# Performance work log

Hardware: AMD Instinct MI355X
Metric: run time of the kernel (lower is better)

## Reference

```python
import jax, jax.numpy as jnp
import numpy as np
import math

V = 50000; E = 300; H = 512; T = 11; P = 18; L = 2048
NHEAD = 2; NLAYERS = 2; NUM_LSTM_LAYERS = 2; FF = E  # TransformerEncoderLayer dim_feedforward=embedding_dim
START, STOP = 0, 1
NEG = -10000.0


def _mk_lstm_params(key, in_dim, hid):
    ks = jax.random.split(key, 4)
    s = 1.0 / math.sqrt(hid)
    return {
        'Wi': jax.random.uniform(ks[0], (4 * hid, in_dim), minval=-s, maxval=s),
        'Wh': jax.random.uniform(ks[1], (4 * hid, hid), minval=-s, maxval=s),
        'bi': jax.random.uniform(ks[2], (4 * hid,), minval=-s, maxval=s),
        'bh': jax.random.uniform(ks[3], (4 * hid,), minval=-s, maxval=s),
    }


def setup_inputs() -> dict:
    key = jax.random.key(0)
    ks = jax.random.split(key, 32)
    sentence = jax.random.randint(ks[0], (L,), 0, V)
    pos_tagging = jax.random.randint(ks[1], (L,), 0, P)
    tf_idf = jax.random.uniform(ks[2], (L,))
    tags = jax.random.randint(ks[3], (L,), 2, T)  # avoid START/STOP as gold tags

    word_embeds = jax.random.normal(ks[4], (V, E)) * 0.1

    in_dim = E + P + 1
    half = H // 2
    lstm = []
    ki = 5
    for layer in range(NUM_LSTM_LAYERS):
        d = in_dim if layer == 0 else H
        lstm.append({'fwd': _mk_lstm_params(ks[ki], d, half), 'bwd': _mk_lstm_params(ks[ki + 1], d, half)})
        ki += 2
    h0 = jax.random.normal(ks[ki], (2 * NUM_LSTM_LAYERS, half)); ki += 1
    c0 = jax.random.normal(ks[ki], (2 * NUM_LSTM_LAYERS, half)); ki += 1

    def dense(k, o, i):
        s = 1.0 / math.sqrt(i)
        k1, k2 = jax.random.split(k)
        return (jax.random.uniform(k1, (o, i), minval=-s, maxval=s),
                jax.random.uniform(k2, (o,), minval=-s, maxval=s))

    tlayers = []
    for _ in range(NLAYERS):
        kk = jax.random.split(ks[ki], 8); ki += 1
        Wqkv, bqkv = dense(kk[0], 3 * H, H)
        Wo, bo = dense(kk[1], H, H)
        W1, b1 = dense(kk[2], FF, H)
        W2, b2 = dense(kk[3], H, FF)
        tlayers.append({
            'Wqkv': Wqkv, 'bqkv': bqkv, 'Wo': Wo, 'bo': bo,
            'W1': W1, 'b1': b1, 'W2': W2, 'b2': b2,
            'g1': jnp.ones((H,)), 'be1': jnp.zeros((H,)),
            'g2': jnp.ones((H,)), 'be2': jnp.zeros((H,)),
        })

    W_tag, b_tag = dense(ks[ki], T, H); ki += 1
    transitions = jax.random.normal(ks[ki], (T, T))
    transitions = transitions.at[START, :].set(NEG).at[:, STOP].set(NEG)

    # flatten transformer params into named entries
    inp = {
        'sentence': sentence, 'pos_tagging': pos_tagging, 'tf_idf': tf_idf, 'tags': tags,
        'word_embeds': word_embeds, 'h0': h0, 'c0': c0,
        'W_tag': W_tag, 'b_tag': b_tag, 'transitions': transitions,
    }
    for li in range(NUM_LSTM_LAYERS):
        for d in ('fwd', 'bwd'):
            for p in ('Wi', 'Wh', 'bi', 'bh'):
                inp[f'lstm{li}_{d}_{p}'] = lstm[li][d][p]
    for li in range(NLAYERS):
        for p, v in tlayers[li].items():
            inp[f't{li}_{p}'] = v
    return inp


def _lstm_dir(x, p, h0, c0, reverse):
    # x: [L, in_dim]
    def step(carry, xt):
        h, c = carry
        g = p['Wi'] @ xt + p['bi'] + p['Wh'] @ h + p['bh']
        i, f, gg, o = jnp.split(g, 4)
        i = jax.nn.sigmoid(i); f = jax.nn.sigmoid(f); o = jax.nn.sigmoid(o)
        c = f * c + i * jnp.tanh(gg)
        h = o * jnp.tanh(c)
        return (h, c), h
    _, hs = jax.lax.scan(step, (h0, c0), x, reverse=reverse)
    return hs  # [L, hid]


def _layernorm(x, g, b):
    m = jnp.mean(x, -1, keepdims=True)
    v = jnp.var(x, -1, keepdims=True)
    return (x - m) / jnp.sqrt(v + 1e-5) * g + b


def _pos_encoding(d_model, max_len):
    position = jnp.arange(max_len, dtype=jnp.float32)[:, None]
    div = jnp.exp(jnp.arange(0, d_model, 2, dtype=jnp.float32) * (-math.log(10000.0) / d_model))
    pe = jnp.zeros((max_len, d_model))
    pe = pe.at[:, 0::2].set(jnp.sin(position * div))
    pe = pe.at[:, 1::2].set(jnp.cos(position * div))
    return pe


def _encoder_layer(x, p, mask):
    # x: [L, H]; post-norm, relu FFN (PyTorch defaults), dropout=eval off
    Lx = x.shape[0]
    qkv = x @ p['Wqkv'].T + p['bqkv']
    q, k, v = jnp.split(qkv, 3, axis=-1)
    dh = H // NHEAD
    q = q.reshape(Lx, NHEAD, dh).transpose(1, 0, 2)
    k = k.reshape(Lx, NHEAD, dh).transpose(1, 0, 2)
    v = v.reshape(Lx, NHEAD, dh).transpose(1, 0, 2)
    scores = jnp.einsum('hqd,hkd->hqk', q, k) / math.sqrt(dh) + mask[None]
    attn = jax.nn.softmax(scores, axis=-1)
    o = jnp.einsum('hqk,hkd->hqd', attn, v).transpose(1, 0, 2).reshape(Lx, H)
    o = o @ p['Wo'].T + p['bo']
    x = _layernorm(x + o, p['g1'], p['be1'])
    ff = jax.nn.relu(x @ p['W1'].T + p['b1']) @ p['W2'].T + p['b2']
    return _layernorm(x + ff, p['g2'], p['be2'])


def _crf_forward(feats, transitions):
    # feats: [L, T]
    init = jnp.full((T,), NEG).at[START].set(0.0)
    def step(fv, feat):
        # next_tag_var[next, prev] = fv[prev] + trans[next, prev] + feat[next]
        m = fv[None, :] + transitions + feat[:, None]
        return jax.nn.logsumexp(m, axis=1), None
    fv, _ = jax.lax.scan(step, init, feats)
    return jax.nn.logsumexp(fv + transitions[STOP])


def _gold_score(feats, tags, transitions):
    ext = jnp.concatenate([jnp.array([START]), tags])
    Lx = feats.shape[0]
    emit = feats[jnp.arange(Lx), ext[1:]].sum()
    trans = transitions[ext[1:], ext[:-1]].sum()
    return emit + trans + transitions[STOP, ext[-1]]


def _forward_feats(sentence, pos_tagging, tf_idf, params):
    Lx = sentence.shape[0]
    embeds = params['word_embeds'][sentence]
    pos = jax.nn.one_hot(pos_tagging, P)
    x = jnp.concatenate([embeds, pos, tf_idf[:, None]], axis=1)  # [L, E+P+1]
    for li in range(NUM_LSTM_LAYERS):
        pf = {k: params[f'lstm{li}_fwd_{k}'] for k in ('Wi', 'Wh', 'bi', 'bh')}
        pb = {k: params[f'lstm{li}_bwd_{k}'] for k in ('Wi', 'Wh', 'bi', 'bh')}
        hf = _lstm_dir(x, pf, params['h0'][2 * li], params['c0'][2 * li], False)
        hb = _lstm_dir(x, pb, params['h0'][2 * li + 1], params['c0'][2 * li + 1], True)
        x = jnp.concatenate([hf, hb], axis=-1)  # [L, H]
    lstm_out = x
    src = lstm_out * math.sqrt(H) + _pos_encoding(H, Lx)
    mask = jnp.where(jnp.tril(jnp.ones((Lx, Lx), bool)), 0.0, -jnp.inf)
    for li in range(NLAYERS):
        p = {k: params[f't{li}_{k}'] for k in ('Wqkv', 'bqkv', 'Wo', 'bo', 'W1', 'b1', 'W2', 'b2', 'g1', 'be1', 'g2', 'be2')}
        src = _encoder_layer(src, p, mask)
    return src @ params['W_tag'].T + params['b_tag']  # [L, T]


def reference(sentence, pos_tagging, tf_idf, tags, word_embeds, h0, c0, W_tag, b_tag, transitions, **params):
    params = dict(params, word_embeds=word_embeds, h0=h0, c0=c0, W_tag=W_tag, b_tag=b_tag)
    feats = _forward_feats(sentence, pos_tagging, tf_idf, params)
    fwd = _crf_forward(feats, transitions)
    gold = _gold_score(feats, tags, transitions)
    return fwd - gold  # neg_log_likelihood scalar
```

## Files before the change

kernel.cpp:

```cpp
#include <hip/hip_runtime.h>
#include <math.h>

typedef unsigned short u16;
typedef unsigned int u32;
typedef _Float16 f16;
typedef f16 f16x2 __attribute__((ext_vector_type(2)));
typedef f16 f16x8 __attribute__((ext_vector_type(8)));
typedef short short8 __attribute__((ext_vector_type(8)));
typedef float f32x4 __attribute__((ext_vector_type(4)));

#define LSEQ 2048
#define NTAG 11

static __device__ __forceinline__ float b2f(u16 u){ union{u32 i; float f;} v; v.i=((u32)u)<<16; return v.f; }
static __device__ __forceinline__ u16 f2b(float f){ union{float fl; u32 i;} v; v.fl=f; u32 r=v.i+0x7fffu+((v.i>>16)&1u); return (u16)(r>>16); }
static u16 h_f2b(float f){ union{float fl; u32 i;} v; v.fl=f; u32 r=v.i+0x7fffu+((v.i>>16)&1u); return (u16)(r>>16); }
static __device__ __forceinline__ float fdot2f(f16x2 a, f16x2 b, float c){
#if __has_builtin(__builtin_amdgcn_fdot2)
  return __builtin_amdgcn_fdot2(a,b,c,false);
#else
  return c + (float)a[0]*(float)b[0] + (float)a[1]*(float)b[1];
#endif
}
static __device__ __forceinline__ float tanh_f(float x){ float e=__expf(2.f*x); return 1.f - 2.f/(e+1.f); }

__global__ __launch_bounds__(256) void cvt2d_k(const float* __restrict__ src, u16* __restrict__ dst,
                                               int rows, int cols, int sld, int dld){
  int i = blockIdx.x*256 + threadIdx.x;
  if (i >= rows*dld) return;
  int r = i/dld, c = i - r*dld;
  float v = (c < cols) ? src[(long)r*sld + c] : 0.f;
  dst[i] = f2b(v);
}

__global__ __launch_bounds__(256) void whpack_k(const float* __restrict__ wh, u32* __restrict__ wall){
  int i = blockIdx.x*256 + threadIdx.x;
  if (i >= 1024*128) return;
  int row = i>>7, c = i&127;
  f16x2 p; p[0] = (f16)wh[row*256 + 2*c]; p[1] = (f16)wh[row*256 + 2*c + 1];
  wall[c*1024 + row] = __builtin_bit_cast(u32, p);
}

__global__ __launch_bounds__(256) void bsum_k(float* __restrict__ out,
    const float* bi0, const float* bh0, const float* bi1, const float* bh1,
    const float* bi2, const float* bh2, const float* bi3, const float* bh3){
  int i = blockIdx.x*256 + threadIdx.x;
  if (i >= 4096) return;
  int c = i>>10, j = i&1023;
  const float* bi = c==0?bi0:c==1?bi1:c==2?bi2:bi3;
  const float* bh = c==0?bh0:c==1?bh1:c==2?bh2:bh3;
  out[i] = bi[j] + bh[j];
}

__global__ void embed_k(const int* __restrict__ sent, const int* __restrict__ pos,
                        const float* __restrict__ tfidf, const float* __restrict__ we,
                        u16* __restrict__ x0h){
  int t = blockIdx.x, c = threadIdx.x;
  float v;
  if (c < 300)      v = we[(long)sent[t]*300 + c];
  else if (c < 318) v = (pos[t] == (c-300)) ? 1.f : 0.f;
  else if (c == 318) v = tfidf[t];
  else               v = 0.f;
  x0h[t*320 + c] = f2b(v);
}

__global__ __launch_bounds__(256) void gemm_k(const u16* __restrict__ A, const u16* __restrict__ B, void* __restrict__ C,
    int M, int N, int K, int lda, int ldb, int ldc,
    long aBS, long bBS, long cBS,
    const float* __restrict__ bias, int flags, int Npad)
{
  int zb = blockIdx.z;
  const u16* Ab = A + (long)zb*aBS;
  const u16* Bb = B + (long)zb*bBS;
  int m0 = blockIdx.y*64, n0 = blockIdx.x*64;
  __shared__ u16 As[64][40], Bs[64][40];
  int tid = threadIdx.x;
  int lane = tid & 63, wv = tid >> 6;
  int srow = tid >> 2, schk = tid & 3;
  int wr = wv >> 1, wc = wv & 1;
  int frow = lane & 15, fk = (lane >> 4) * 8;
  const u16* pa = Ab + (long)(m0+srow)*lda + schk*8;
  bool bval = (n0 + srow) < N;
  const u16* pb = Bb + (long)(n0+srow)*ldb + schk*8;
  f32x4 acc[2][2];
  #pragma unroll
  for (int mi=0;mi<2;mi++)
  #pragma unroll
  for (int ni=0;ni<2;ni++) acc[mi][ni] = (f32x4){0.f,0.f,0.f,0.f};

  for (int k0=0; k0<K; k0+=32){
    uint4 av = *(const uint4*)pa; pa += 32;
    uint4 bv; if (bval) bv = *(const uint4*)pb; else { bv.x=0u; bv.y=0u; bv.z=0u; bv.w=0u; }
    pb += 32;
    *(uint4*)&As[srow][schk*8] = av;
    *(uint4*)&Bs[srow][schk*8] = bv;
    __syncthreads();
    short8 a[2], b[2];
    a[0] = *(const short8*)&As[wr*32      + frow][fk];
    a[1] = *(const short8*)&As[wr*32 + 16 + frow][fk];
    b[0] = *(const short8*)&Bs[wc*32      + frow][fk];
    b[1] = *(const short8*)&Bs[wc*32 + 16 + frow][fk];
    #pragma unroll
    for (int mi=0;mi<2;mi++)
    #pragma unroll
    for (int ni=0;ni<2;ni++)
      acc[mi][ni] = __builtin_amdgcn_mfma_f32_16x16x32_bf16(a[mi], b[ni], acc[mi][ni], 0,0,0);
    __syncthreads();
  }
  int mrow = (lane>>4)*4, ncol = lane&15;
  #pragma unroll
  for (int mi=0;mi<2;mi++)
  #pragma unroll
  for (int ni=0;ni<2;ni++){
    int nn = n0 + wc*32 + ni*16 + ncol;
    #pragma unroll
    for (int j=0;j<4;j++){
      int mm = m0 + wr*32 + mi*16 + mrow + j;
      long ci = (long)zb*cBS + (long)mm*ldc + nn;
      if (nn < N){
        float v = acc[mi][ni][j];
        if (flags & 1) v += bias[nn];
        if (flags & 2) v = fmaxf(v, 0.f);
        if (flags & 4) ((u16*)C)[ci] = f2b(v); else ((float*)C)[ci] = v;
      } else if (nn < Npad){
        if (flags & 4) ((u16*)C)[ci] = 0; else ((float*)C)[ci] = 0.f;
      }
    }
  }
}

__global__ __launch_bounds__(512, 1) void lstm_k(
    const float* __restrict__ preF, const float* __restrict__ preB,
    const u32* __restrict__ wallF, const u32* __restrict__ wallB,
    const float* __restrict__ h0, const float* __restrict__ c0, int sbase,
    float* __restrict__ outf, u16* __restrict__ outh)
{
  int dir = blockIdx.x;
  const float* pre = dir ? preB  : preF;
  const u32* wall  = dir ? wallB : wallF;
  __shared__ __align__(16) f16 hl[256];
  __shared__ float gl[1024];
  int tid = threadIdx.x;
  int rowA = tid, rowB = tid + 512;

  u32 wA[128], wB[128];
  #pragma unroll
  for (int c=0;c<128;c++) wA[c] = wall[c*1024 + rowA];
  #pragma unroll
  for (int c=0;c<128;c++) wB[c] = wall[c*1024 + rowB];
  float cst = 0.f;
  if (tid < 256){
    hl[tid] = (f16)h0[(sbase+dir)*256 + tid];
    cst = c0[(sbase+dir)*256 + tid];
  }
  __syncthreads();

  for (int s=0; s<LSEQ; s++){
    int t = dir ? (LSEQ-1-s) : s;
    float pvA = pre[(long)t*1024 + rowA];
    float pvB = pre[(long)t*1024 + rowB];
    float a0=0.f,a1=0.f,b0=0.f,b1=0.f;
    #pragma unroll
    for (int v=0; v<16; v++){
      f16x8 hv = *(const f16x8*)&hl[v*8];
      const f16x2* h2 = (const f16x2*)&hv;
      #pragma unroll
      for (int j=0;j<4;j++){
        f16x2 wa = __builtin_bit_cast(f16x2, wA[4*v+j]);
        f16x2 wb = __builtin_bit_cast(f16x2, wB[4*v+j]);
        if (j&1){ a1 = fdot2f(wa,h2[j],a1); b1 = fdot2f(wb,h2[j],b1); }
        else    { a0 = fdot2f(wa,h2[j],a0); b0 = fdot2f(wb,h2[j],b0); }
      }
    }
    gl[rowA] = a0+a1+pvA;
    gl[rowB] = b0+b1+pvB;
    __syncthreads();
    if (tid < 256){
      float gi=gl[tid], gf=gl[tid+256], gg=gl[tid+512], go=gl[tid+768];
      float ii=1.f/(1.f+__expf(-gi));
      float ff=1.f/(1.f+__expf(-gf));
      float oo=1.f/(1.f+__expf(-go));
      cst = ff*cst + ii*tanh_f(gg);
      float h = oo*tanh_f(cst);
      hl[tid] = (f16)h;
      long oi = (long)t*512 + dir*256 + tid;
      outf[oi] = h; outh[oi] = f2b(h);
    }
    __syncthreads();
  }
}

__global__ __launch_bounds__(512) void posenc_k(const float* __restrict__ xin, float* __restrict__ srcf, u16* __restrict__ srch){
  int t = blockIdx.x, d = threadIdx.x;
  long i = (long)t*512 + d;
  float v = xin[i] * 22.627416997969522f;
  float dv = __expf(-(float)(d & ~1) * 0.017988946039015984f);
  float ang = (float)t * dv;
  v += (d & 1) ? cosf(ang) : sinf(ang);
  srcf[i] = v; srch[i] = f2b(v);
}

__global__ __launch_bounds__(512) void trv_k(const u16* __restrict__ qkv, u16* __restrict__ vt){
  __shared__ u16 tile[64][65];
  int h = blockIdx.z;
  int lb = blockIdx.x*64, db = blockIdx.y*64;
  int tx = threadIdx.x, ty = threadIdx.y;
  #pragma unroll
  for (int j=0;j<8;j++){
    int l = lb + ty + j*8;
    tile[ty + j*8][tx] = qkv[(long)l*1536 + 1024 + h*256 + db + tx];
  }
  __syncthreads();
  #pragma unroll
  for (int j=0;j<8;j++){
    int d = db + ty + j*8;
    vt[((long)h*256 + d)*2048 + lb + tx] = tile[tx][ty + j*8];
  }
}

__global__ __launch_bounds__(256) void softmax_k(const float* __restrict__ sc, u16* __restrict__ P){
  int q = blockIdx.x;
  const float* row = sc + (long)q*LSEQ;
  u16* prow = P + (long)q*LSEQ;
  int tid = threadIdx.x, lane = tid&63, wv = tid>>6;
  int n = q + 1;
  __shared__ float sm[4], ss[4];
  float mx = -1e30f;
  for (int c=tid; c<n; c+=256) mx = fmaxf(mx, row[c]);
  #pragma unroll
  for (int o=32;o;o>>=1) mx = fmaxf(mx, __shfl_xor(mx,o));
  if (!lane) sm[wv] = mx;
  __syncthreads();
  float mxs = fmaxf(fmaxf(sm[0],sm[1]),fmaxf(sm[2],sm[3])) * 0.0625f;
  float sum = 0.f;
  for (int c=tid; c<n; c+=256) sum += __expf(row[c]*0.0625f - mxs);
  #pragma unroll
  for (int o=32;o;o>>=1) sum += __shfl_xor(sum,o);
  if (!lane) ss[wv] = sum;
  __syncthreads();
  float inv = 1.f/(ss[0]+ss[1]+ss[2]+ss[3]);
  for (int c=tid; c<LSEQ; c+=256){
    float pv = (c<n) ? __expf(row[c]*0.0625f - mxs)*inv : 0.f;
    prow[c] = f2b(pv);
  }
}

__global__ __launch_bounds__(256) void addln_k(const float* __restrict__ x, const float* __restrict__ y,
                                               const float* __restrict__ g, const float* __restrict__ be,
                                               float* __restrict__ outf, u16* __restrict__ outh){
  int t = blockIdx.x, tid = threadIdx.x, lane = tid&63, wv = tid>>6;
  long base = (long)t*512;
  float v0 = x[base+tid]     + y[base+tid];
  float v1 = x[base+256+tid] + y[base+256+tid];
  float s = v0+v1, qq = v0*v0 + v1*v1;
  __shared__ float rs[4], rq[4];
  #pragma unroll
  for (int o=32;o;o>>=1){ s += __shfl_xor(s,o); qq += __shfl_xor(qq,o); }
  if (!lane){ rs[wv]=s; rq[wv]=qq; }
  __syncthreads();
  s  = rs[0]+rs[1]+rs[2]+rs[3];
  qq = rq[0]+rq[1]+rq[2]+rq[3];
  float mean = s*(1.f/512.f);
  float var  = qq*(1.f/512.f) - mean*mean;
  float inv = rsqrtf(var + 1e-5f);
  float o0 = (v0-mean)*inv*g[tid]     + be[tid];
  float o1 = (v1-mean)*inv*g[tid+256] + be[tid+256];
  outf[base+tid]     = o0; outh[base+tid]     = f2b(o0);
  outf[base+256+tid] = o1; outh[base+256+tid] = f2b(o1);
}

__global__ __launch_bounds__(256) void crf_k(const float* __restrict__ feats, const float* __restrict__ trans,
                                             const int* __restrict__ tags, u32* __restrict__ out){
  __shared__ float red[256];
  int tid = threadIdx.x;
  float acc = 0.f;
  for (int t=tid; t<LSEQ; t+=256){
    int tg = tags[t];
    int pv = t ? tags[t-1] : 0;
    acc += feats[t*NTAG + tg] + trans[tg*NTAG + pv];
  }
  red[tid] = acc; __syncthreads();
  for (int s=128; s; s>>=1){ if (tid < s) red[tid] += red[tid+s]; __syncthreads(); }
  float gold = red[0] + trans[1*NTAG + tags[LSEQ-1]];
  if (tid >= 64) return;
  int n = tid;
  bool act = n < NTAG;
  float Trow[NTAG];
  #pragma unroll
  for (int p=0;p<NTAG;p++) Trow[p] = act ? trans[n*NTAG + p] : 0.f;
  float fv = (n==0) ? 0.f : -10000.f;
  float feat = act ? feats[n] : 0.f;
  for (int t=0; t<LSEQ; t++){
    float featN = (t+1 < LSEQ) ? (act ? feats[(t+1)*NTAG + n] : 0.f) : 0.f;
    float v[NTAG]; float mx = -1e30f;
    #pragma unroll
    for (int p=0;p<NTAG;p++){
      float fvp = __shfl(fv, p);
      v[p] = fvp + Trow[p];
      mx = fmaxf(mx, v[p]);
    }
    float sum = 0.f;
    #pragma unroll
    for (int p=0;p<NTAG;p++) sum += __expf(v[p] - mx);
    fv = feat + mx + __logf(sum);
    feat = featN;
  }
  float tv = act ? fv + trans[1*NTAG + n] : -1e30f;
  float m2 = tv;
  #pragma unroll
  for (int o=32;o;o>>=1) m2 = fmaxf(m2, __shfl_xor(m2,o));
  float se = __expf(tv - m2);
  #pragma unroll
  for (int o=32;o;o>>=1) se += __shfl_xor(se,o);
  float fwd = m2 + __logf(se);
  if (tid == 0){
    u32 bits = (u32)f2b(fwd - gold);
    out[0] = (bits << 16) | bits;
  }
}

extern "C" void kernel_launch(void* const* d_in, const int* in_sizes, int n_in,
                              void* d_out, int out_size, void* d_ws, size_t ws_size,
                              hipStream_t stream) {
  (void)in_sizes; (void)n_in; (void)out_size;
  const int*   sent  = (const int*)  d_in[0];
  const int*   pos   = (const int*)  d_in[1];
  const float* tfidf = (const float*)d_in[2];
  const int*   tags  = (const int*)  d_in[3];
  const float* we    = (const float*)d_in[4];
  const float* h0    = (const float*)d_in[5];
  const float* c0    = (const float*)d_in[6];
  const float* Wtag  = (const float*)d_in[7];
  const float* btag  = (const float*)d_in[8];
  const float* trans = (const float*)d_in[9];
  const float* lWi[4] = {(const float*)d_in[10],(const float*)d_in[14],(const float*)d_in[18],(const float*)d_in[22]};
  const float* lWh[4] = {(const float*)d_in[11],(const float*)d_in[15],(const float*)d_in[19],(const float*)d_in[23]};
  const float* lbi[4] = {(const float*)d_in[12],(const float*)d_in[16],(const float*)d_in[20],(const float*)d_in[24]};
  const float* lbh[4] = {(const float*)d_in[13],(const float*)d_in[17],(const float*)d_in[21],(const float*)d_in[25]};
  const float *Wqkv[2], *bqkv[2], *Wo[2], *bo[2], *W1[2], *b1[2], *W2[2], *b2[2], *g1[2], *be1[2], *g2[2], *be2[2];
  for (int li=0; li<2; li++){
    const float** slots[12] = {&Wqkv[li],&bqkv[li],&Wo[li],&bo[li],&W1[li],&b1[li],&W2[li],&b2[li],&g1[li],&be1[li],&g2[li],&be2[li]};
    for (int k=0;k<12;k++) *slots[k] = (const float*)d_in[26 + li*12 + k];
  }

  auto wdiag = [&](float v){
    u16 u = h_f2b(v);
    unsigned char b0 = (unsigned char)(u & 0xFF), b1 = (unsigned char)(u >> 8);
    char* p = (char*)d_out;
    (void)hipMemsetAsync(p+0, b0, 1, stream);
    (void)hipMemsetAsync(p+1, b1, 1, stream);
    (void)hipMemsetAsync(p+2, b0, 1, stream);
    (void)hipMemsetAsync(p+3, b1, 1, stream);
  };
  (void)hipGetLastError();
  wdiag(2.0f);

  char* base = (char*)d_ws; size_t off = 0;
  auto alc = [&](size_t bytes)->char*{ char* p = base + off; off = (off + bytes + 255) & ~(size_t)255; return p; };

  u16* Wi0fH = (u16*)alc((size_t)1024*320*2);
  u16* Wi0bH = (u16*)alc((size_t)1024*320*2);
  u16* Wi1fH = (u16*)alc((size_t)1024*512*2);
  u16* Wi1bH = (u16*)alc((size_t)1024*512*2);
  u16* WqkvH[2] = {(u16*)alc((size_t)1536*512*2), (u16*)alc((size_t)1536*512*2)};
  u16* WoH[2]   = {(u16*)alc((size_t)512*512*2),  (u16*)alc((size_t)512*512*2)};
  u16* W1H[2]   = {(u16*)alc((size_t)300*512*2),  (u16*)alc((size_t)300*512*2)};
  u16* W2H[2]   = {(u16*)alc((size_t)512*320*2),  (u16*)alc((size_t)512*320*2)};
  u16* WtagH    = (u16*)alc((size_t)11*512*2);
  u32* walls[4];
  for (int c=0;c<4;c++) walls[c] = (u32*)alc((size_t)128*1024*4);
  float* bsums = (float*)alc((size_t)4*1024*4);
  u16* x0h = (u16*)alc((size_t)2048*320*2);
  float* preF = (float*)alc((size_t)2048*1024*4);
  float* preB = (float*)alc((size_t)2048*1024*4);
  float* scoresF = preF;
  float* xaf = (float*)alc((size_t)2048*512*4);
  u16*   xah = (u16*)  alc((size_t)2048*512*2);
  float* xbf = (float*)alc((size_t)2048*512*4);
  u16*   xbh = (u16*)  alc((size_t)2048*512*2);
  float* srcf = (float*)alc((size_t)2048*512*4);
  u16*   srch = (u16*)  alc((size_t)2048*512*2);
  u16* qkvh = (u16*)alc((size_t)2048*1536*2);
  u16* vth  = (u16*)alc((size_t)512*2048*2);
  u16* Pb   = (u16*)alc((size_t)2*2048*2048*2);
  u16* aoh  = (u16*)alc((size_t)2048*512*2);
  float* tmpf = (float*)alc((size_t)2048*512*4);
  u16* ff1h = (u16*)alc((size_t)2048*320*2);
  float* feats = (float*)alc((size_t)2048*NTAG*4);

  if (off > ws_size){ wdiag(-999.0f); return; }

  int stage_fail = 0;
  auto chk = [&](int stage)->bool{
    hipError_t e = hipGetLastError();
    if (e != hipSuccess){
      wdiag(-(float)(stage*1000 + ((int)e % 1000)));
      stage_fail = 1;
      return false;
    }
    return true;
  };

  auto cvt = [&](const float* s, u16* d, int r, int c, int sld, int dld){
    cvt2d_k<<<(r*dld+255)/256, 256, 0, stream>>>(s, d, r, c, sld, dld);
  };
  auto gemm = [&](const u16* A, const u16* B, void* C, int M, int N, int K,
                  int lda, int ldb, int ldc, long aBS, long bBS, long cBS,
                  const float* bias, int flags, int batch){
    dim3 g(((unsigned)N+63)/64, ((unsigned)M+63)/64, batch);
    gemm_k<<<g, 256, 0, stream>>>(A, B, C, M, N, K, lda, ldb, ldc, aBS, bBS, cBS, bias, flags, N);
  };

  cvt(lWi[0], Wi0fH, 1024, 319, 319, 320);
  cvt(lWi[1], Wi0bH, 1024, 319, 319, 320);
  cvt(lWi[2], Wi1fH, 1024, 512, 512, 512);
  cvt(lWi[3], Wi1bH, 1024, 512, 512, 512);
  for (int li=0; li<2; li++){
    cvt(Wqkv[li], WqkvH[li], 1536, 512, 512, 512);
    cvt(Wo[li],   WoH[li],   512, 512, 512, 512);
    cvt(W1[li],   W1H[li],   300, 512, 512, 512);
    cvt(W2[li],   W2H[li],   512, 300, 300, 320);
  }
  cvt(Wtag, WtagH, 11, 512, 512, 512);
  for (int c=0;c<4;c++) whpack_k<<<512, 256, 0, stream>>>(lWh[c], walls[c]);
  bsum_k<<<16, 256, 0, stream>>>(bsums, lbi[0],lbh[0], lbi[1],lbh[1], lbi[2],lbh[2], lbi[3],lbh[3]);
  embed_k<<<2048, 320, 0, stream>>>(sent, pos, tfidf, we, x0h);
  if (!chk(1)) return;

  gemm(x0h, Wi0fH, preF, 2048, 1024, 320, 320, 320, 1024, 0,0,0, bsums + 0,    1, 1);
  gemm(x0h, Wi0bH, preB, 2048, 1024, 320, 320, 320, 1024, 0,0,0, bsums + 1024, 1, 1);
  if (!chk(2)) return;
  lstm_k<<<2, 512, 0, stream>>>(preF, preB, walls[0], walls[1], h0, c0, 0, xaf, xah);
  if (!chk(3)) return;
  wdiag(3.0f);

  gemm(xah, Wi1fH, preF, 2048, 1024, 512, 512, 512, 1024, 0,0,0, bsums + 2048, 1, 1);
  gemm(xah, Wi1bH, preB, 2048, 1024, 512, 512, 512, 1024, 0,0,0, bsums + 3072, 1, 1);
  lstm_k<<<2, 512, 0, stream>>>(preF, preB, walls[2], walls[3], h0, c0, 2, xbf, xbh);
  if (!chk(4)) return;

  posenc_k<<<2048, 512, 0, stream>>>(xbf, srcf, srch);
  if (!chk(5)) return;
  wdiag(4.0f);

  for (int li=0; li<2; li++){
    gemm(srch, WqkvH[li], qkvh, 2048, 1536, 512, 512, 512, 1536, 0,0,0, bqkv[li], 1|4, 1);
    trv_k<<<dim3(32,4,2), dim3(64,8), 0, stream>>>(qkvh, vth);
    for (int h=0; h<2; h++){
      gemm(qkvh + h*256, qkvh + 512 + h*256, scoresF, 2048, 2048, 256, 1536, 1536, 2048, 0,0,0, nullptr, 0, 1);
      softmax_k<<<2048, 256, 0, stream>>>(scoresF, Pb + (long)h*2048*2048);
    }
    gemm(Pb, vth, aoh, 2048, 256, 2048, 2048, 2048, 512,
         (long)2048*2048, (long)256*2048, 256, nullptr, 4, 2);
    gemm(aoh, WoH[li], tmpf, 2048, 512, 512, 512, 512, 512, 0,0,0, bo[li], 1, 1);
    addln_k<<<2048, 256, 0, stream>>>(srcf, tmpf, g1[li], be1[li], srcf, srch);
    gemm(srch, W1H[li], ff1h, 2048, 300, 512, 512, 512, 320, 0,0,0, b1[li], 1|2|4, 1);
    gemm(ff1h, W2H[li], tmpf, 2048, 512, 320, 320, 320, 512, 0,0,0, b2[li], 1, 1);
    addln_k<<<2048, 256, 0, stream>>>(srcf, tmpf, g2[li], be2[li], srcf, srch);
    if (!chk(6 + li)) return;
  }

  gemm(srch, WtagH, feats, 2048, NTAG, 512, 512, 512, NTAG, 0,0,0, btag, 1, 1);
  crf_k<<<1, 256, 0, stream>>>(feats, trans, tags, (u32*)d_out);
  if (!chk(8)) return;
  (void)stage_fail;
}
```

Measured before the change: 4.735 ms.

## Use MFMA for LSTM recurrent matvec and prefetch gate preactivations

The LSTM recurrence now computes the Wh·h product with 16x16x32 f16 MFMA instructions instead of per-thread fdot2 loops. The weights are held in registers in an MFMA A-operand layout, and the preactivation loads are prefetched one step ahead by the gate threads. Softmax now caches its exponentials in shared memory rather than recomputing them, and the positional encoding switches to the fast __sinf/__cosf intrinsics. The matvec wastes most of the MFMA output columns because B is a broadcast vector, and the register pressure of the held weight fragments is a risk.

```diff
diff --git a/kernel.cpp b/kernel.cpp
--- a/kernel.cpp
+++ b/kernel.cpp
@@ -15,13 +15,6 @@
 static __device__ __forceinline__ float b2f(u16 u){ union{u32 i; float f;} v; v.i=((u32)u)<<16; return v.f; }
 static __device__ __forceinline__ u16 f2b(float f){ union{float fl; u32 i;} v; v.fl=f; u32 r=v.i+0x7fffu+((v.i>>16)&1u); return (u16)(r>>16); }
 static u16 h_f2b(float f){ union{float fl; u32 i;} v; v.fl=f; u32 r=v.i+0x7fffu+((v.i>>16)&1u); return (u16)(r>>16); }
-static __device__ __forceinline__ float fdot2f(f16x2 a, f16x2 b, float c){
-#if __has_builtin(__builtin_amdgcn_fdot2)
-  return __builtin_amdgcn_fdot2(a,b,c,false);
-#else
-  return c + (float)a[0]*(float)b[0] + (float)a[1]*(float)b[1];
-#endif
-}
 static __device__ __forceinline__ float tanh_f(float x){ float e=__expf(2.f*x); return 1.f - 2.f/(e+1.f); }
 
 __global__ __launch_bounds__(256) void cvt2d_k(const float* __restrict__ src, u16* __restrict__ dst,
@@ -33,12 +26,9 @@
   dst[i] = f2b(v);
 }
 
-__global__ __launch_bounds__(256) void whpack_k(const float* __restrict__ wh, u32* __restrict__ wall){
+__global__ __launch_bounds__(256) void cvt16_k(const float* __restrict__ src, f16* __restrict__ dst, int n){
   int i = blockIdx.x*256 + threadIdx.x;
-  if (i >= 1024*128) return;
-  int row = i>>7, c = i&127;
-  f16x2 p; p[0] = (f16)wh[row*256 + 2*c]; p[1] = (f16)wh[row*256 + 2*c + 1];
-  wall[c*1024 + row] = __builtin_bit_cast(u32, p);
+  if (i < n) dst[i] = (f16)src[i];
 }
 
 __global__ __launch_bounds__(256) void bsum_k(float* __restrict__ out,
@@ -129,62 +119,79 @@
   }
 }
 
-__global__ __launch_bounds__(512, 1) void lstm_k(
+__global__ __launch_bounds__(512, 2) void lstm_m(
     const float* __restrict__ preF, const float* __restrict__ preB,
-    const u32* __restrict__ wallF, const u32* __restrict__ wallB,
+    const f16* __restrict__ whF, const f16* __restrict__ whB,
     const float* __restrict__ h0, const float* __restrict__ c0, int sbase,
     float* __restrict__ outf, u16* __restrict__ outh)
 {
   int dir = blockIdx.x;
-  const float* pre = dir ? preB  : preF;
-  const u32* wall  = dir ? wallB : wallF;
+  const float* pre = dir ? preB : preF;
+  const f16*  wh   = dir ? whB  : whF;
   __shared__ __align__(16) f16 hl[256];
   __shared__ float gl[1024];
   int tid = threadIdx.x;
-  int rowA = tid, rowB = tid + 512;
-
-  u32 wA[128], wB[128];
-  #pragma unroll
-  for (int c=0;c<128;c++) wA[c] = wall[c*1024 + rowA];
-  #pragma unroll
-  for (int c=0;c<128;c++) wB[c] = wall[c*1024 + rowB];
+  int lane = tid & 63, w = tid >> 6;
+  int arow = lane & 15;
+  int akoff = (lane >> 4) * 8;
+
+  f16x8 A[8][8];
+  #pragma unroll
+  for (int i=0;i<8;i++)
+    #pragma unroll
+    for (int kk=0;kk<8;kk++)
+      A[i][kk] = *(const f16x8*)&wh[(long)(w*128 + i*16 + arow)*256 + kk*32 + akoff];
+
   float cst = 0.f;
+  float pv0=0.f, pv1=0.f, pv2=0.f, pv3=0.f;
   if (tid < 256){
     hl[tid] = (f16)h0[(sbase+dir)*256 + tid];
     cst = c0[(sbase+dir)*256 + tid];
+    long tb = (long)(dir ? (LSEQ-1) : 0) * 1024;
+    pv0 = pre[tb + tid]; pv1 = pre[tb + 256 + tid];
+    pv2 = pre[tb + 512 + tid]; pv3 = pre[tb + 768 + tid];
   }
   __syncthreads();
 
   for (int s=0; s<LSEQ; s++){
     int t = dir ? (LSEQ-1-s) : s;
-    float pvA = pre[(long)t*1024 + rowA];
-    float pvB = pre[(long)t*1024 + rowB];
-    float a0=0.f,a1=0.f,b0=0.f,b1=0.f;
-    #pragma unroll
-    for (int v=0; v<16; v++){
-      f16x8 hv = *(const f16x8*)&hl[v*8];
-      const f16x2* h2 = (const f16x2*)&hv;
+    f16x8 B[8];
+    #pragma unroll
+    for (int kk=0;kk<8;kk++) B[kk] = *(const f16x8*)&hl[kk*32 + akoff];
+    f32x4 C[8];
+    #pragma unroll
+    for (int i=0;i<8;i++) C[i] = (f32x4){0.f,0.f,0.f,0.f};
+    #pragma unroll
+    for (int kk=0;kk<8;kk++)
       #pragma unroll
-      for (int j=0;j<4;j++){
-        f16x2 wa = __builtin_bit_cast(f16x2, wA[4*v+j]);
-        f16x2 wb = __builtin_bit_cast(f16x2, wB[4*v+j]);
-        if (j&1){ a1 = fdot2f(wa,h2[j],a1); b1 = fdot2f(wb,h2[j],b1); }
-        else    { a0 = fdot2f(wa,h2[j],a0); b0 = fdot2f(wb,h2[j],b0); }
+      for (int i=0;i<8;i++)
+        C[i] = __builtin_amdgcn_mfma_f32_16x16x32_f16(A[i][kk], B[kk], C[i], 0, 0, 0);
+    #pragma unroll
+    for (int i=0;i<8;i++){
+      if ((lane & 15) == i){
+        int rb = w*128 + i*16 + (lane>>4)*4;
+        gl[rb+0] = C[i][0]; gl[rb+1] = C[i][1]; gl[rb+2] = C[i][2]; gl[rb+3] = C[i][3];
       }
     }
-    gl[rowA] = a0+a1+pvA;
-    gl[rowB] = b0+b1+pvB;
     __syncthreads();
     if (tid < 256){
-      float gi=gl[tid], gf=gl[tid+256], gg=gl[tid+512], go=gl[tid+768];
-      float ii=1.f/(1.f+__expf(-gi));
-      float ff=1.f/(1.f+__expf(-gf));
-      float oo=1.f/(1.f+__expf(-go));
+      float gi = gl[tid]       + pv0;
+      float gf = gl[tid + 256] + pv1;
+      float gg = gl[tid + 512] + pv2;
+      float go = gl[tid + 768] + pv3;
+      float ii = 1.f/(1.f+__expf(-gi));
+      float ff = 1.f/(1.f+__expf(-gf));
+      float oo = 1.f/(1.f+__expf(-go));
       cst = ff*cst + ii*tanh_f(gg);
       float h = oo*tanh_f(cst);
       hl[tid] = (f16)h;
       long oi = (long)t*512 + dir*256 + tid;
       outf[oi] = h; outh[oi] = f2b(h);
+      if (s + 1 < LSEQ){
+        long tb = (long)(dir ? (t-1) : (t+1)) * 1024;
+        pv0 = pre[tb + tid]; pv1 = pre[tb + 256 + tid];
+        pv2 = pre[tb + 512 + tid]; pv3 = pre[tb + 768 + tid];
+      }
     }
     __syncthreads();
   }
@@ -196,7 +203,7 @@
   float v = xin[i] * 22.627416997969522f;
   float dv = __expf(-(float)(d & ~1) * 0.017988946039015984f);
   float ang = (float)t * dv;
-  v += (d & 1) ? cosf(ang) : sinf(ang);
+  v += (d & 1) ? __cosf(ang) : __sinf(ang);
   srcf[i] = v; srch[i] = f2b(v);
 }
 
@@ -225,6 +232,7 @@
   int tid = threadIdx.x, lane = tid&63, wv = tid>>6;
   int n = q + 1;
   __shared__ float sm[4], ss[4];
+  __shared__ float ex[LSEQ];
   float mx = -1e30f;
   for (int c=tid; c<n; c+=256) mx = fmaxf(mx, row[c]);
   #pragma unroll
@@ -233,16 +241,17 @@
   __syncthreads();
   float mxs = fmaxf(fmaxf(sm[0],sm[1]),fmaxf(sm[2],sm[3])) * 0.0625f;
   float sum = 0.f;
-  for (int c=tid; c<n; c+=256) sum += __expf(row[c]*0.0625f - mxs);
+  for (int c=tid; c<n; c+=256){
+    float e = __expf(row[c]*0.0625f - mxs);
+    ex[c] = e; sum += e;
+  }
   #pragma unroll
   for (int o=32;o;o>>=1) sum += __shfl_xor(sum,o);
   if (!lane) ss[wv] = sum;
   __syncthreads();
   float inv = 1.f/(ss[0]+ss[1]+ss[2]+ss[3]);
-  for (int c=tid; c<LSEQ; c+=256){
-    float pv = (c<n) ? __expf(row[c]*0.0625f - mxs)*inv : 0.f;
-    prow[c] = f2b(pv);
-  }
+  for (int c=tid; c<LSEQ; c+=256)
+    prow[c] = (c<n) ? f2b(ex[c]*inv) : (u16)0;
 }
 
 __global__ __launch_bounds__(256) void addln_k(const float* __restrict__ x, const float* __restrict__ y,
@@ -353,7 +362,6 @@
     (void)hipMemsetAsync(p+3, b1, 1, stream);
   };
   (void)hipGetLastError();
-  wdiag(2.0f);
 
   char* base = (char*)d_ws; size_t off = 0;
   auto alc = [&](size_t bytes)->char*{ char* p = base + off; off = (off + bytes + 255) & ~(size_t)255; return p; };
@@ -367,8 +375,8 @@
   u16* W1H[2]   = {(u16*)alc((size_t)300*512*2),  (u16*)alc((size_t)300*512*2)};
   u16* W2H[2]   = {(u16*)alc((size_t)512*320*2),  (u16*)alc((size_t)512*320*2)};
   u16* WtagH    = (u16*)alc((size_t)11*512*2);
-  u32* walls[4];
-  for (int c=0;c<4;c++) walls[c] = (u32*)alc((size_t)128*1024*4);
+  f16* whf[4];
+  for (int c=0;c<4;c++) whf[c] = (f16*)alc((size_t)1024*256*2);
   float* bsums = (float*)alc((size_t)4*1024*4);
   u16* x0h = (u16*)alc((size_t)2048*320*2);
   float* preF = (float*)alc((size_t)2048*1024*4);
@@ -390,14 +398,9 @@
 
   if (off > ws_size){ wdiag(-999.0f); return; }
 
-  int stage_fail = 0;
   auto chk = [&](int stage)->bool{
     hipError_t e = hipGetLastError();
-    if (e != hipSuccess){
-      wdiag(-(float)(stage*1000 + ((int)e % 1000)));
-      stage_fail = 1;
-      return false;
-    }
+    if (e != hipSuccess){ wdiag(-(float)(stage*1000 + ((int)e % 1000))); return false; }
     return true;
   };
 
@@ -422,7 +425,7 @@
     cvt(W2[li],   W2H[li],   512, 300, 300, 320);
   }
   cvt(Wtag, WtagH, 11, 512, 512, 512);
-  for (int c=0;c<4;c++) whpack_k<<<512, 256, 0, stream>>>(lWh[c], walls[c]);
+  for (int c=0;c<4;c++) cvt16_k<<<1024, 256, 0, stream>>>(lWh[c], whf[c], 1024*256);
   bsum_k<<<16, 256, 0, stream>>>(bsums, lbi[0],lbh[0], lbi[1],lbh[1], lbi[2],lbh[2], lbi[3],lbh[3]);
   embed_k<<<2048, 320, 0, stream>>>(sent, pos, tfidf, we, x0h);
   if (!chk(1)) return;
@@ -430,18 +433,16 @@
   gemm(x0h, Wi0fH, preF, 2048, 1024, 320, 320, 320, 1024, 0,0,0, bsums + 0,    1, 1);
   gemm(x0h, Wi0bH, preB, 2048, 1024, 320, 320, 320, 1024, 0,0,0, bsums + 1024, 1, 1);
   if (!chk(2)) return;
-  lstm_k<<<2, 512, 0, stream>>>(preF, preB, walls[0], walls[1], h0, c0, 0, xaf, xah);
+  lstm_m<<<2, 512, 0, stream>>>(preF, preB, whf[0], whf[1], h0, c0, 0, xaf, xah);
   if (!chk(3)) return;
-  wdiag(3.0f);
 
   gemm(xah, Wi1fH, preF, 2048, 1024, 512, 512, 512, 1024, 0,0,0, bsums + 2048, 1, 1);
   gemm(xah, Wi1bH, preB, 2048, 1024, 512, 512, 512, 1024, 0,0,0, bsums + 3072, 1, 1);
-  lstm_k<<<2, 512, 0, stream>>>(preF, preB, walls[2], walls[3], h0, c0, 2, xbf, xbh);
+  lstm_m<<<2, 512, 0, stream>>>(preF, preB, whf[2], whf[3], h0, c0, 2, xbf, xbh);
   if (!chk(4)) return;
 
   posenc_k<<<2048, 512, 0, stream>>>(xbf, srcf, srch);
   if (!chk(5)) return;
-  wdiag(4.0f);
 
   for (int li=0; li<2; li++){
     gemm(srch, WqkvH[li], qkvh, 2048, 1536, 512, 512, 512, 1536, 0,0,0, bqkv[li], 1|4, 1);
@@ -463,5 +464,4 @@
   gemm(srch, WtagH, feats, 2048, NTAG, 512, 512, 512, NTAG, 0,0,0, btag, 1, 1);
   crf_k<<<1, 256, 0, stream>>>(feats, trans, tags, (u32*)d_out);
   if (!chk(8)) return;
-  (void)stage_fail;
-}
+}
```

Result: slower. 17.17 ms (+262.7%).

## Split LSTM recurrent weights between registers and global loads, cache softmax exponentials

Applied to the files above, without the earlier changes.

The LSTM recurrent kernel now keeps only the first half of each row's packed recurrent weights in registers and re-reads the rest from global memory (L2) on every timestep, loosening the launch bound to allow two blocks per CU. This trades the per-step latency of the serial recurrence against register pressure and possible spills. Softmax caches its exponentials in shared memory so they are not recomputed, and positional encoding uses fast intrinsic sin/cos. Several wdiag diagnostic memset calls are also removed from the host path.

```diff
diff --git a/kernel.cpp b/kernel.cpp
--- a/kernel.cpp
+++ b/kernel.cpp
@@ -11,6 +11,7 @@
 
 #define LSEQ 2048
 #define NTAG 11
+#define RES 64
 
 static __device__ __forceinline__ float b2f(u16 u){ union{u32 i; float f;} v; v.i=((u32)u)<<16; return v.f; }
 static __device__ __forceinline__ u16 f2b(float f){ union{float fl; u32 i;} v; v.fl=f; u32 r=v.i+0x7fffu+((v.i>>16)&1u); return (u16)(r>>16); }
@@ -129,25 +130,26 @@
   }
 }
 
-__global__ __launch_bounds__(512, 1) void lstm_k(
+__global__ __launch_bounds__(512, 2) void lstm_h(
     const float* __restrict__ preF, const float* __restrict__ preB,
     const u32* __restrict__ wallF, const u32* __restrict__ wallB,
     const float* __restrict__ h0, const float* __restrict__ c0, int sbase,
     float* __restrict__ outf, u16* __restrict__ outh)
 {
   int dir = blockIdx.x;
-  const float* pre = dir ? preB  : preF;
+  const float* pre = dir ? preB : preF;
   const u32* wall  = dir ? wallB : wallF;
   __shared__ __align__(16) f16 hl[256];
   __shared__ float gl[1024];
   int tid = threadIdx.x;
   int rowA = tid, rowB = tid + 512;
 
-  u32 wA[128], wB[128];
-  #pragma unroll
-  for (int c=0;c<128;c++) wA[c] = wall[c*1024 + rowA];
-  #pragma unroll
-  for (int c=0;c<128;c++) wB[c] = wall[c*1024 + rowB];
+  u32 wA[RES], wB[RES];
+  #pragma unroll
+  for (int c=0;c<RES;c++) wA[c] = wall[c*1024 + rowA];
+  #pragma unroll
+  for (int c=0;c<RES;c++) wB[c] = wall[c*1024 + rowB];
+
   float cst = 0.f;
   if (tid < 256){
     hl[tid] = (f16)h0[(sbase+dir)*256 + tid];
@@ -161,13 +163,26 @@
     float pvB = pre[(long)t*1024 + rowB];
     float a0=0.f,a1=0.f,b0=0.f,b1=0.f;
     #pragma unroll
-    for (int v=0; v<16; v++){
+    for (int v=0; v<RES/4; v++){
       f16x8 hv = *(const f16x8*)&hl[v*8];
       const f16x2* h2 = (const f16x2*)&hv;
       #pragma unroll
       for (int j=0;j<4;j++){
         f16x2 wa = __builtin_bit_cast(f16x2, wA[4*v+j]);
         f16x2 wb = __builtin_bit_cast(f16x2, wB[4*v+j]);
+        if (j&1){ a1 = fdot2f(wa,h2[j],a1); b1 = fdot2f(wb,h2[j],b1); }
+        else    { a0 = fdot2f(wa,h2[j],a0); b0 = fdot2f(wb,h2[j],b0); }
+      }
+    }
+    #pragma unroll
+    for (int v=0; v<(128-RES)/4; v++){
+      f16x8 hv = *(const f16x8*)&hl[2*RES + v*8];
+      const f16x2* h2 = (const f16x2*)&hv;
+      #pragma unroll
+      for (int j=0;j<4;j++){
+        int c = RES + 4*v + j;
+        f16x2 wa = __builtin_bit_cast(f16x2, wall[c*1024 + rowA]);
+        f16x2 wb = __builtin_bit_cast(f16x2, wall[c*1024 + rowB]);
         if (j&1){ a1 = fdot2f(wa,h2[j],a1); b1 = fdot2f(wb,h2[j],b1); }
         else    { a0 = fdot2f(wa,h2[j],a0); b0 = fdot2f(wb,h2[j],b0); }
       }
@@ -196,7 +211,7 @@
   float v = xin[i] * 22.627416997969522f;
   float dv = __expf(-(float)(d & ~1) * 0.017988946039015984f);
   float ang = (float)t * dv;
-  v += (d & 1) ? cosf(ang) : sinf(ang);
+  v += (d & 1) ? __cosf(ang) : __sinf(ang);
   srcf[i] = v; srch[i] = f2b(v);
 }
 
@@ -225,6 +240,7 @@
   int tid = threadIdx.x, lane = tid&63, wv = tid>>6;
   int n = q + 1;
   __shared__ float sm[4], ss[4];
+  __shared__ float ex[LSEQ];
   float mx = -1e30f;
   for (int c=tid; c<n; c+=256) mx = fmaxf(mx, row[c]);
   #pragma unroll
@@ -233,16 +249,17 @@
   __syncthreads();
   float mxs = fmaxf(fmaxf(sm[0],sm[1]),fmaxf(sm[2],sm[3])) * 0.0625f;
   float sum = 0.f;
-  for (int c=tid; c<n; c+=256) sum += __expf(row[c]*0.0625f - mxs);
+  for (int c=tid; c<n; c+=256){
+    float e = __expf(row[c]*0.0625f - mxs);
+    ex[c] = e; sum += e;
+  }
   #pragma unroll
   for (int o=32;o;o>>=1) sum += __shfl_xor(sum,o);
   if (!lane) ss[wv] = sum;
   __syncthreads();
   float inv = 1.f/(ss[0]+ss[1]+ss[2]+ss[3]);
-  for (int c=tid; c<LSEQ; c+=256){
-    float pv = (c<n) ? __expf(row[c]*0.0625f - mxs)*inv : 0.f;
-    prow[c] = f2b(pv);
-  }
+  for (int c=tid; c<LSEQ; c+=256)
+    prow[c] = (c<n) ? f2b(ex[c]*inv) : (u16)0;
 }
 
 __global__ __launch_bounds__(256) void addln_k(const float* __restrict__ x, const float* __restrict__ y,
@@ -353,7 +370,6 @@
     (void)hipMemsetAsync(p+3, b1, 1, stream);
   };
   (void)hipGetLastError();
-  wdiag(2.0f);
 
   char* base = (char*)d_ws; size_t off = 0;
   auto alc = [&](size_t bytes)->char*{ char* p = base + off; off = (off + bytes + 255) & ~(size_t)255; return p; };
@@ -390,14 +406,9 @@
 
   if (off > ws_size){ wdiag(-999.0f); return; }
 
-  int stage_fail = 0;
   auto chk = [&](int stage)->bool{
     hipError_t e = hipGetLastError();
-    if (e != hipSuccess){
-      wdiag(-(float)(stage*1000 + ((int)e % 1000)));
-      stage_fail = 1;
-      return false;
-    }
+    if (e != hipSuccess){ wdiag(-(float)(stage*1000 + ((int)e % 1000))); return false; }
     return true;
   };
 
@@ -430,18 +441,16 @@
   gemm(x0h, Wi0fH, preF, 2048, 1024, 320, 320, 320, 1024, 0,0,0, bsums + 0,    1, 1);
   gemm(x0h, Wi0bH, preB, 2048, 1024, 320, 320, 320, 1024, 0,0,0, bsums + 1024, 1, 1);
   if (!chk(2)) return;
-  lstm_k<<<2, 512, 0, stream>>>(preF, preB, walls[0], walls[1], h0, c0, 0, xaf, xah);
+  lstm_h<<<2, 512, 0, stream>>>(preF, preB, walls[0], walls[1], h0, c0, 0, xaf, xah);
   if (!chk(3)) return;
-  wdiag(3.0f);
 
   gemm(xah, Wi1fH, preF, 2048, 1024, 512, 512, 512, 1024, 0,0,0, bsums + 2048, 1, 1);
   gemm(xah, Wi1bH, preB, 2048, 1024, 512, 512, 512, 1024, 0,0,0, bsums + 3072, 1, 1);
-  lstm_k<<<2, 512, 0, stream>>>(preF, preB, walls[2], walls[3], h0, c0, 2, xbf, xbh);
+  lstm_h<<<2, 512, 0, stream>>>(preF, preB, walls[2], walls[3], h0, c0, 2, xbf, xbh);
   if (!chk(4)) return;
 
   posenc_k<<<2048, 512, 0, stream>>>(xbf, srcf, srch);
   if (!chk(5)) return;
-  wdiag(4.0f);
 
   for (int li=0; li<2; li++){
     gemm(srch, WqkvH[li], qkvh, 2048, 1536, 512, 512, 512, 1536, 0,0,0, bqkv[li], 1|4, 1);
@@ -463,5 +472,4 @@
   gemm(srch, WtagH, feats, 2048, NTAG, 512, 512, 512, NTAG, 0,0,0, btag, 1, 1);
   crf_k<<<1, 256, 0, stream>>>(feats, trans, tags, (u32*)d_out);
   if (!chk(8)) return;
-  (void)stage_fail;
-}
+}
```

Result: slower. 14.52 ms (+206.7%).
